# Kernel optimization log

Measured on AMD Instinct MI355X. Metric: run time of the kernel, lower is better.

## Reference

```python
import jax, jax.numpy as jnp
import numpy as np

# NF4 codebook (QLoRA): 16 quantile values of a standard normal, normalized to [-1, 1]
NF4_TABLE = jnp.array([
    -1.0, -0.6961928009986877, -0.5250730514526367, -0.39491748809814453,
    -0.28444138169288635, -0.18477343022823334, -0.09105003625154495, 0.0,
    0.07958029955625534, 0.16093020141124725, 0.24611230194568634,
    0.33791524171829224, 0.44070982933044434, 0.5626170039176941,
    0.7229568362236328, 1.0], dtype=jnp.float32)

IN_DIM = 4096
OUT_DIM = 4096
RANK = 16
ALPHA = 32.0
BLOCK = 64  # NF4 quantization block size along the flattened weight


def setup_inputs() -> dict:
    key = jax.random.key(0)
    k1, k2, k3, k4, k5 = jax.random.split(key, 5)
    x = jax.random.normal(k1, (4, 2048, IN_DIM), dtype=jnp.float32)
    # 4-bit codes into NF4_TABLE, stored unpacked as int32
    w_codes = jax.random.randint(k2, (OUT_DIM, IN_DIM), 0, 16, dtype=jnp.int32)
    # per-block absmax scales (positive)
    w_scales = jax.random.uniform(k3, (OUT_DIM, IN_DIM // BLOCK), dtype=jnp.float32) * 0.02 + 1e-3
    # lora_a: kaiming-uniform-ish scale; lora_b: nonzero for testability (original inits to zeros)
    lora_a = jax.random.normal(k4, (RANK, IN_DIM), dtype=jnp.float32) * (1.0 / np.sqrt(IN_DIM))
    lora_b = jax.random.normal(k5, (OUT_DIM, RANK), dtype=jnp.float32) * 0.01
    return {"x": x, "w_codes": w_codes, "w_scales": w_scales, "lora_a": lora_a, "lora_b": lora_b}


def _dequant_nf4(w_codes, w_scales):
    # codes [O, I] -> dequantized weight [O, I]
    w = NF4_TABLE[w_codes]                                   # [O, I]
    w = w.reshape(OUT_DIM, IN_DIM // BLOCK, BLOCK) * w_scales[:, :, None]
    return w.reshape(OUT_DIM, IN_DIM)


def reference(x, w_codes, w_scales, lora_a, lora_b):
    # base: frozen NF4 linear (dequantize then matmul), no bias
    w = _dequant_nf4(w_codes, w_scales)                      # [O, I]
    base = jnp.einsum('bsi,oi->bso', x, w)                   # [B, S, O]
    # LoRA path: dropout p=0.0 -> identity; scale alpha / rank
    ax = jnp.einsum('bsi,ri->bsr', x, lora_a)                # [B, S, r]
    lora = jnp.einsum('bsr,or->bso', ax, lora_b)             # [B, S, O]
    return base + (ALPHA / RANK) * lora
```

## Files before the change

### kernel.cpp

```cpp
#include <hip/hip_runtime.h>
#include <hip/hip_bf16.h>


#define IN_DIM  4096
#define OUT_DIM 4096
#define RANK    16
#define M_TOK   8192
#define LORA_SCALE 2.0f

typedef __bf16 bf16_t;
typedef bf16_t bf16x8 __attribute__((ext_vector_type(8)));
typedef float  f32x4  __attribute__((ext_vector_type(4)));

__device__ __constant__ float NF4_TAB[16] = {
    -1.0f, -0.6961928009986877f, -0.5250730514526367f, -0.39491748809814453f,
    -0.28444138169288635f, -0.18477343022823334f, -0.09105003625154495f, 0.0f,
    0.07958029955625534f, 0.16093020141124725f, 0.24611230194568634f,
    0.33791524171829224f, 0.44070982933044434f, 0.5626170039176941f,
    0.7229568362236328f, 1.0f};

__global__ __launch_bounds__(256) void prep_w(
    const int* __restrict__ codes, const float* __restrict__ scales,
    const float* __restrict__ la, const float* __restrict__ lb,
    bf16_t* __restrict__ W)
{
    __shared__ float nf4s[16];
    __shared__ float lbs[4][16];
    const int o0 = blockIdx.x * 4;
    const int tid = threadIdx.x;
    if (tid < 64) lbs[tid >> 4][tid & 15] = lb[(o0 + (tid >> 4)) * RANK + (tid & 15)] * LORA_SCALE;
    else if (tid < 80) nf4s[tid - 64] = NF4_TAB[tid - 64];
    __syncthreads();

    #pragma unroll
    for (int it = 0; it < 2; ++it) {
        const int i0 = (it * 256 + tid) * 8;
        float w[4][8];
        #pragma unroll
        for (int oo = 0; oo < 4; ++oo) {
            const size_t base = (size_t)(o0 + oo) * IN_DIM + i0;
            int4 c0 = *(const int4*)(codes + base);
            int4 c1 = *(const int4*)(codes + base + 4);
            const float sc = scales[(o0 + oo) * (IN_DIM / 64) + (i0 >> 6)];
            w[oo][0] = nf4s[c0.x] * sc; w[oo][1] = nf4s[c0.y] * sc;
            w[oo][2] = nf4s[c0.z] * sc; w[oo][3] = nf4s[c0.w] * sc;
            w[oo][4] = nf4s[c1.x] * sc; w[oo][5] = nf4s[c1.y] * sc;
            w[oo][6] = nf4s[c1.z] * sc; w[oo][7] = nf4s[c1.w] * sc;
        }
        #pragma unroll
        for (int r = 0; r < RANK; ++r) {
            float4 a0 = *(const float4*)(la + r * IN_DIM + i0);
            float4 a1 = *(const float4*)(la + r * IN_DIM + i0 + 4);
            #pragma unroll
            for (int oo = 0; oo < 4; ++oo) {
                const float b = lbs[oo][r];
                w[oo][0] += b * a0.x; w[oo][1] += b * a0.y;
                w[oo][2] += b * a0.z; w[oo][3] += b * a0.w;
                w[oo][4] += b * a1.x; w[oo][5] += b * a1.y;
                w[oo][6] += b * a1.z; w[oo][7] += b * a1.w;
            }
        }
        #pragma unroll
        for (int oo = 0; oo < 4; ++oo) {
            bf16x8 v;
            #pragma unroll
            for (int j = 0; j < 8; ++j) v[j] = (bf16_t)w[oo][j];
            *(bf16x8*)(W + (size_t)(o0 + oo) * IN_DIM + i0) = v;
        }
    }
}

__global__ __launch_bounds__(256) void cast_x(
    const float* __restrict__ x, bf16_t* __restrict__ y, int n8)
{
    const int stride = gridDim.x * blockDim.x;
    for (int i = blockIdx.x * blockDim.x + threadIdx.x; i < n8; i += stride) {
        const size_t e = (size_t)i * 8;
        float4 a = *(const float4*)(x + e);
        float4 b = *(const float4*)(x + e + 4);
        bf16x8 v;
        v[0] = (bf16_t)a.x; v[1] = (bf16_t)a.y; v[2] = (bf16_t)a.z; v[3] = (bf16_t)a.w;
        v[4] = (bf16_t)b.x; v[5] = (bf16_t)b.y; v[6] = (bf16_t)b.z; v[7] = (bf16_t)b.w;
        *(bf16x8*)(y + e) = v;
    }
}

__global__ __launch_bounds__(512, 2) void gemm_bt(
    const bf16_t* __restrict__ A, const bf16_t* __restrict__ B,
    float* __restrict__ C)
{
    __shared__ __align__(128) char lds[131072];

    const int tid  = threadIdx.x;
    const int wave = tid >> 6;
    const int lane = tid & 63;

    const int flat = blockIdx.y * gridDim.x + blockIdx.x;
    const int swz  = (flat & 7) * 64 + (flat >> 3);
    const int bx = swz & 15;
    const int by = swz >> 4;
    const int m0 = by * 256;
    const int n0 = bx * 256;

    const int wr = wave >> 2;
    const int wc = wave & 3;

    f32x4 acc[8][4];
    #pragma unroll
    for (int i = 0; i < 8; ++i)
        #pragma unroll
        for (int j = 0; j < 4; ++j) acc[i][j] = (f32x4)0.0f;

    const int frow = lane & 15;
    const int fch  = lane >> 4;
    const int fxor = (fch ^ ((frow >> 1) & 3)) << 4;
    const int aoff = (wr * 128 + frow) * 64 + fxor;
    const int boff = (wc * 64  + frow) * 64 + fxor;

    const int d0 = tid * 16, d1 = 8192 + tid * 16;
    const int sr0 = d0 >> 6, sr1 = d1 >> 6;
    const int sg0 = ((d0 >> 4) & 3) ^ ((sr0 >> 1) & 3);
    const int sg1 = ((d1 >> 4) & 3) ^ ((sr1 >> 1) & 3);
    const char* gA = (const char*)A;
    const char* gB = (const char*)B;

    bf16x8 fAe[8], fAo[8], fBe[2], fBo[2];

#define RD_A2(FA, SL, KH, J0) do {                                             \
    const char* b_ = lds + (SL) * 65536 + (KH) * 16384;                        \
    FA[(J0)]     = *(const bf16x8*)(b_ + aoff + (J0) * 1024);                  \
    FA[(J0) + 1] = *(const bf16x8*)(b_ + aoff + ((J0) + 1) * 1024);            \
} while (0)

#define RD_B(FB, SL, KH, NH) do {                                              \
    const char* b_ = lds + (SL) * 65536 + 32768 + (KH) * 16384;                \
    FB[0] = *(const bf16x8*)(b_ + boff + (NH) * 2048);                         \
    FB[1] = *(const bf16x8*)(b_ + boff + (NH) * 2048 + 1024);                  \
} while (0)

#define STG1(OPI, KH_, SL, T) do {                                             \
    const char* g_  = (OPI) ? gB : gA;                                         \
    const int   r0_ = (OPI) ? n0 : m0;                                         \
    const size_t ko_ = (size_t)(T) * 128 + (KH_) * 64;                         \
    const char* s0_ = g_ + (size_t)(r0_ + sr0) * 8192 + ko_ + (sg0 << 4);      \
    const char* s1_ = g_ + (size_t)(r0_ + sr1) * 8192 + ko_ + (sg1 << 4);      \
    char* db_ = lds + (SL) * 65536 + (OPI) * 32768 + (KH_) * 16384 + wave * 1024; \
    __builtin_amdgcn_global_load_lds(                                          \
        (const __attribute__((address_space(1))) void*)s0_,                    \
        (__attribute__((address_space(3))) void*)db_, 16, 0, 0);               \
    __builtin_amdgcn_global_load_lds(                                          \
        (const __attribute__((address_space(1))) void*)s1_,                    \
        (__attribute__((address_space(3))) void*)(db_ + 8192), 16, 0, 0);      \
} while (0)

#define MM4(FA, F0, FB, BI, NH) do {                                           \
    _Pragma("unroll")                                                          \
    for (int f_ = 0; f_ < 4; ++f_)                                             \
        acc[(F0) + f_][(NH) * 2 + (BI)] =                                      \
            __builtin_amdgcn_mfma_f32_16x16x32_bf16(                           \
                FA[(F0) + f_], FB[BI], acc[(F0) + f_][(NH) * 2 + (BI)], 0, 0, 0); \
} while (0)

#define PHASE(SOP, SKH, SSL, ST, CHK, FA, FB, NH, RD1, RD2, RD3) do {          \
    STG1(SOP, SKH, SSL, ST);                                                   \
    if (CHK) { asm volatile("s_waitcnt vmcnt(6)" ::: "memory"); }              \
    __builtin_amdgcn_sched_barrier(0);                                         \
    __builtin_amdgcn_s_barrier();                                              \
    __builtin_amdgcn_s_setprio(1);                                             \
    MM4(FA, 0, FB, 0, NH);                                                     \
    RD1;                                                                       \
    MM4(FA, 0, FB, 1, NH);                                                     \
    RD2;                                                                       \
    MM4(FA, 4, FB, 0, NH);                                                     \
    RD3;                                                                       \
    MM4(FA, 4, FB, 1, NH);                                                     \
    __builtin_amdgcn_s_setprio(0);                                             \
    __builtin_amdgcn_s_barrier();                                              \
} while (0)

    STG1(0, 0, 0, 0); STG1(1, 0, 0, 0); STG1(0, 1, 0, 0); STG1(1, 1, 0, 0);
    STG1(0, 0, 1, 1); STG1(1, 0, 1, 1); STG1(0, 1, 1, 1);
    asm volatile("s_waitcnt vmcnt(6)" ::: "memory");
    __builtin_amdgcn_s_barrier();
    RD_A2(fAe, 0, 0, 0); RD_A2(fAe, 0, 0, 2);
    RD_A2(fAe, 0, 0, 4); RD_A2(fAe, 0, 0, 6);
    RD_B(fBe, 0, 0, 0);

    for (int i = 0; i < 32; ++i) {
        const int tY  = 2 * i + 1;
        const int tS0 = (2 * i + 2) & 63;
        const int tS1 = (2 * i + 3) & 63;
        PHASE(1, 1, 1, tY,  0, fAe, fBe, 0,
              RD_A2(fAo, 0, 1, 0), RD_A2(fAo, 0, 1, 2), RD_B(fBo, 0, 0, 1));
        PHASE(0, 0, 0, tS0, 1, fAe, fBo, 1,
              RD_A2(fAo, 0, 1, 4), RD_A2(fAo, 0, 1, 6), RD_B(fBe, 0, 1, 0));
        PHASE(1, 0, 0, tS0, 0, fAo, fBe, 0,
              RD_A2(fAe, 1, 0, 0), RD_A2(fAe, 1, 0, 2), RD_B(fBo, 0, 1, 1));
        PHASE(0, 1, 0, tS0, 1, fAo, fBo, 1,
              RD_A2(fAe, 1, 0, 4), RD_A2(fAe, 1, 0, 6), RD_B(fBe, 1, 0, 0));
        PHASE(1, 1, 0, tS0, 0, fAe, fBe, 0,
              RD_A2(fAo, 1, 1, 0), RD_A2(fAo, 1, 1, 2), RD_B(fBo, 1, 0, 1));
        PHASE(0, 0, 1, tS1, 1, fAe, fBo, 1,
              RD_A2(fAo, 1, 1, 4), RD_A2(fAo, 1, 1, 6), RD_B(fBe, 1, 1, 0));
        PHASE(1, 0, 1, tS1, 0, fAo, fBe, 0,
              RD_A2(fAe, 0, 0, 0), RD_A2(fAe, 0, 0, 2), RD_B(fBo, 1, 1, 1));
        PHASE(0, 1, 1, tS1, 1, fAo, fBo, 1,
              RD_A2(fAe, 0, 0, 4), RD_A2(fAe, 0, 0, 6), RD_B(fBe, 0, 0, 0));
    }

    const int crow = (lane >> 4) * 4;
    const int ccol = lane & 15;
    #pragma unroll
    for (int i = 0; i < 8; ++i) {
        #pragma unroll
        for (int j = 0; j < 4; ++j) {
            const int mb = m0 + wr * 128 + i * 16 + crow;
            const int nb = n0 + wc * 64 + j * 16 + ccol;
            #pragma unroll
            for (int r = 0; r < 4; ++r)
                C[(size_t)(mb + r) * OUT_DIM + nb] = acc[i][j][r];
        }
    }
#undef RD_A2
#undef RD_B
#undef STG1
#undef MM4
#undef PHASE
}

extern "C" void kernel_launch(void* const* d_in, const int* in_sizes, int n_in,
                              void* d_out, int out_size, void* d_ws, size_t ws_size,
                              hipStream_t stream) {
    const float* x      = (const float*)d_in[0];
    const int*   codes  = (const int*)d_in[1];
    const float* scales = (const float*)d_in[2];
    const float* la     = (const float*)d_in[3];
    const float* lb     = (const float*)d_in[4];
    float* out = (float*)d_out;

    bf16_t* W  = (bf16_t*)d_ws;
    bf16_t* xb = (bf16_t*)((char*)d_ws + (size_t)OUT_DIM * IN_DIM * 2);

    prep_w<<<OUT_DIM / 4, 256, 0, stream>>>(codes, scales, la, lb, W);
    cast_x<<<2048, 256, 0, stream>>>(x, xb, (M_TOK * IN_DIM) / 8);

    dim3 grid(OUT_DIM / 256, M_TOK / 256);
    gemm_bt<<<grid, 512, 0, stream>>>(xb, W, out);
}
```

Before: 293.7 us.

## Switch GEMM to 32x32x16 MFMA and merge weight prep with x cast

The GEMM inner loop now issues 32x32x16 bf16 MFMAs into 16-wide accumulators instead of 16x16x32 tiles, which changes the LDS fragment addressing and the output store mapping. The aim is fewer MFMA issues and better operand reuse per instruction. Separately, the NF4 weight dequant/LoRA-fold kernel and the x-to-bf16 cast are merged into one launch so they share the GPU and one launch overhead is dropped. The main risks are a wrong fragment or k-ordering mapping for the larger MFMA, and coalescing changes in the store epilogue.

```diff
diff --git a/kernel.cpp b/kernel.cpp
--- a/kernel.cpp
+++ b/kernel.cpp
@@ -9,8 +9,8 @@
 #define LORA_SCALE 2.0f
 
 typedef __bf16 bf16_t;
-typedef bf16_t bf16x8 __attribute__((ext_vector_type(8)));
-typedef float  f32x4  __attribute__((ext_vector_type(4)));
+typedef bf16_t bf16x8  __attribute__((ext_vector_type(8)));
+typedef float  f32x16  __attribute__((ext_vector_type(16)));
 
 __device__ __constant__ float NF4_TAB[16] = {
     -1.0f, -0.6961928009986877f, -0.5250730514526367f, -0.39491748809814453f,
@@ -19,69 +19,70 @@
     0.33791524171829224f, 0.44070982933044434f, 0.5626170039176941f,
     0.7229568362236328f, 1.0f};
 
-__global__ __launch_bounds__(256) void prep_w(
+__global__ __launch_bounds__(256) void prep_all(
+    const float* __restrict__ x,
     const int* __restrict__ codes, const float* __restrict__ scales,
     const float* __restrict__ la, const float* __restrict__ lb,
-    bf16_t* __restrict__ W)
+    bf16_t* __restrict__ W, bf16_t* __restrict__ xb)
 {
-    __shared__ float nf4s[16];
-    __shared__ float lbs[4][16];
-    const int o0 = blockIdx.x * 4;
     const int tid = threadIdx.x;
-    if (tid < 64) lbs[tid >> 4][tid & 15] = lb[(o0 + (tid >> 4)) * RANK + (tid & 15)] * LORA_SCALE;
-    else if (tid < 80) nf4s[tid - 64] = NF4_TAB[tid - 64];
-    __syncthreads();
-
-    #pragma unroll
-    for (int it = 0; it < 2; ++it) {
-        const int i0 = (it * 256 + tid) * 8;
-        float w[4][8];
+    if (blockIdx.x < 1024) {
+        __shared__ float nf4s[16];
+        __shared__ float lbs[4][16];
+        const int o0 = blockIdx.x * 4;
+        if (tid < 64) lbs[tid >> 4][tid & 15] = lb[(o0 + (tid >> 4)) * RANK + (tid & 15)] * LORA_SCALE;
+        else if (tid < 80) nf4s[tid - 64] = NF4_TAB[tid - 64];
+        __syncthreads();
+
         #pragma unroll
-        for (int oo = 0; oo < 4; ++oo) {
-            const size_t base = (size_t)(o0 + oo) * IN_DIM + i0;
-            int4 c0 = *(const int4*)(codes + base);
-            int4 c1 = *(const int4*)(codes + base + 4);
-            const float sc = scales[(o0 + oo) * (IN_DIM / 64) + (i0 >> 6)];
-            w[oo][0] = nf4s[c0.x] * sc; w[oo][1] = nf4s[c0.y] * sc;
-            w[oo][2] = nf4s[c0.z] * sc; w[oo][3] = nf4s[c0.w] * sc;
-            w[oo][4] = nf4s[c1.x] * sc; w[oo][5] = nf4s[c1.y] * sc;
-            w[oo][6] = nf4s[c1.z] * sc; w[oo][7] = nf4s[c1.w] * sc;
+        for (int it = 0; it < 2; ++it) {
+            const int i0 = (it * 256 + tid) * 8;
+            float w[4][8];
+            #pragma unroll
+            for (int oo = 0; oo < 4; ++oo) {
+                const size_t base = (size_t)(o0 + oo) * IN_DIM + i0;
+                int4 c0 = *(const int4*)(codes + base);
+                int4 c1 = *(const int4*)(codes + base + 4);
+                const float sc = scales[(o0 + oo) * (IN_DIM / 64) + (i0 >> 6)];
+                w[oo][0] = nf4s[c0.x] * sc; w[oo][1] = nf4s[c0.y] * sc;
+                w[oo][2] = nf4s[c0.z] * sc; w[oo][3] = nf4s[c0.w] * sc;
+                w[oo][4] = nf4s[c1.x] * sc; w[oo][5] = nf4s[c1.y] * sc;
+                w[oo][6] = nf4s[c1.z] * sc; w[oo][7] = nf4s[c1.w] * sc;
+            }
+            #pragma unroll
+            for (int r = 0; r < RANK; ++r) {
+                float4 a0 = *(const float4*)(la + r * IN_DIM + i0);
+                float4 a1 = *(const float4*)(la + r * IN_DIM + i0 + 4);
+                #pragma unroll
+                for (int oo = 0; oo < 4; ++oo) {
+                    const float b = lbs[oo][r];
+                    w[oo][0] += b * a0.x; w[oo][1] += b * a0.y;
+                    w[oo][2] += b * a0.z; w[oo][3] += b * a0.w;
+                    w[oo][4] += b * a1.x; w[oo][5] += b * a1.y;
+                    w[oo][6] += b * a1.z; w[oo][7] += b * a1.w;
+                }
+            }
+            #pragma unroll
+            for (int oo = 0; oo < 4; ++oo) {
+                bf16x8 v;
+                #pragma unroll
+                for (int j = 0; j < 8; ++j) v[j] = (bf16_t)w[oo][j];
+                *(bf16x8*)(W + (size_t)(o0 + oo) * IN_DIM + i0) = v;
+            }
         }
-        #pragma unroll
-        for (int r = 0; r < RANK; ++r) {
-            float4 a0 = *(const float4*)(la + r * IN_DIM + i0);
-            float4 a1 = *(const float4*)(la + r * IN_DIM + i0 + 4);
-            #pragma unroll
-            for (int oo = 0; oo < 4; ++oo) {
-                const float b = lbs[oo][r];
-                w[oo][0] += b * a0.x; w[oo][1] += b * a0.y;
-                w[oo][2] += b * a0.z; w[oo][3] += b * a0.w;
-                w[oo][4] += b * a1.x; w[oo][5] += b * a1.y;
-                w[oo][6] += b * a1.z; w[oo][7] += b * a1.w;
-            }
+    } else {
+        const int bid = blockIdx.x - 1024;
+        const int n8 = (M_TOK * IN_DIM) / 8;
+        const int stride = 2048 * 256;
+        for (int i = bid * 256 + tid; i < n8; i += stride) {
+            const size_t e = (size_t)i * 8;
+            float4 a = *(const float4*)(x + e);
+            float4 b = *(const float4*)(x + e + 4);
+            bf16x8 v;
+            v[0] = (bf16_t)a.x; v[1] = (bf16_t)a.y; v[2] = (bf16_t)a.z; v[3] = (bf16_t)a.w;
+            v[4] = (bf16_t)b.x; v[5] = (bf16_t)b.y; v[6] = (bf16_t)b.z; v[7] = (bf16_t)b.w;
+            *(bf16x8*)(xb + e) = v;
         }
-        #pragma unroll
-        for (int oo = 0; oo < 4; ++oo) {
-            bf16x8 v;
-            #pragma unroll
-            for (int j = 0; j < 8; ++j) v[j] = (bf16_t)w[oo][j];
-            *(bf16x8*)(W + (size_t)(o0 + oo) * IN_DIM + i0) = v;
-        }
-    }
-}
-
-__global__ __launch_bounds__(256) void cast_x(
-    const float* __restrict__ x, bf16_t* __restrict__ y, int n8)
-{
-    const int stride = gridDim.x * blockDim.x;
-    for (int i = blockIdx.x * blockDim.x + threadIdx.x; i < n8; i += stride) {
-        const size_t e = (size_t)i * 8;
-        float4 a = *(const float4*)(x + e);
-        float4 b = *(const float4*)(x + e + 4);
-        bf16x8 v;
-        v[0] = (bf16_t)a.x; v[1] = (bf16_t)a.y; v[2] = (bf16_t)a.z; v[3] = (bf16_t)a.w;
-        v[4] = (bf16_t)b.x; v[5] = (bf16_t)b.y; v[6] = (bf16_t)b.z; v[7] = (bf16_t)b.w;
-        *(bf16x8*)(y + e) = v;
     }
 }
 
@@ -105,17 +106,19 @@
     const int wr = wave >> 2;
     const int wc = wave & 3;
 
-    f32x4 acc[8][4];
+    f32x16 acc[4][2];
     #pragma unroll
-    for (int i = 0; i < 8; ++i)
+    for (int i = 0; i < 4; ++i)
         #pragma unroll
-        for (int j = 0; j < 4; ++j) acc[i][j] = (f32x4)0.0f;
-
-    const int frow = lane & 15;
-    const int fch  = lane >> 4;
-    const int fxor = (fch ^ ((frow >> 1) & 3)) << 4;
-    const int aoff = (wr * 128 + frow) * 64 + fxor;
-    const int boff = (wc * 64  + frow) * 64 + fxor;
+        for (int j = 0; j < 2; ++j) acc[i][j] = (f32x16)0.0f;
+
+    const int l31  = lane & 31;
+    const int hi   = lane >> 5;
+    const int xorv = (l31 >> 1) & 3;
+    const int cs0  = ((0 + hi) ^ xorv) << 4;
+    const int cs1  = ((2 + hi) ^ xorv) << 4;
+    const int base_a = (wr * 128 + l31) * 64;
+    const int base_b = (wc * 64  + l31) * 64;
 
     const int d0 = tid * 16, d1 = 8192 + tid * 16;
     const int sr0 = d0 >> 6, sr1 = d1 >> 6;
@@ -127,15 +130,17 @@
     bf16x8 fAe[8], fAo[8], fBe[2], fBo[2];
 
 #define RD_A2(FA, SL, KH, J0) do {                                             \
-    const char* b_ = lds + (SL) * 65536 + (KH) * 16384;                        \
-    FA[(J0)]     = *(const bf16x8*)(b_ + aoff + (J0) * 1024);                  \
-    FA[(J0) + 1] = *(const bf16x8*)(b_ + aoff + ((J0) + 1) * 1024);            \
+    const char* b_ = lds + (SL) * 65536 + (KH) * 16384 + base_a               \
+                     + ((J0) >> 1) * 2048;                                     \
+    FA[(J0)]     = *(const bf16x8*)(b_ + cs0);                                 \
+    FA[(J0) + 1] = *(const bf16x8*)(b_ + cs1);                                 \
 } while (0)
 
 #define RD_B(FB, SL, KH, NH) do {                                              \
-    const char* b_ = lds + (SL) * 65536 + 32768 + (KH) * 16384;                \
-    FB[0] = *(const bf16x8*)(b_ + boff + (NH) * 2048);                         \
-    FB[1] = *(const bf16x8*)(b_ + boff + (NH) * 2048 + 1024);                  \
+    const char* b_ = lds + (SL) * 65536 + 32768 + (KH) * 16384 + base_b       \
+                     + (NH) * 2048;                                            \
+    FB[0] = *(const bf16x8*)(b_ + cs0);                                        \
+    FB[1] = *(const bf16x8*)(b_ + cs1);                                        \
 } while (0)
 
 #define STG1(OPI, KH_, SL, T) do {                                             \
@@ -153,12 +158,11 @@
         (__attribute__((address_space(3))) void*)(db_ + 8192), 16, 0, 0);      \
 } while (0)
 
-#define MM4(FA, F0, FB, BI, NH) do {                                           \
-    _Pragma("unroll")                                                          \
-    for (int f_ = 0; f_ < 4; ++f_)                                             \
-        acc[(F0) + f_][(NH) * 2 + (BI)] =                                      \
-            __builtin_amdgcn_mfma_f32_16x16x32_bf16(                           \
-                FA[(F0) + f_], FB[BI], acc[(F0) + f_][(NH) * 2 + (BI)], 0, 0, 0); \
+#define MM2(FA, FB, I, NH) do {                                                \
+    acc[I][NH] = __builtin_amdgcn_mfma_f32_32x32x16_bf16(                      \
+        FA[2 * (I)], FB[0], acc[I][NH], 0, 0, 0);                              \
+    acc[I][NH] = __builtin_amdgcn_mfma_f32_32x32x16_bf16(                      \
+        FA[2 * (I) + 1], FB[1], acc[I][NH], 0, 0, 0);                          \
 } while (0)
 
 #define PHASE(SOP, SKH, SSL, ST, CHK, FA, FB, NH, RD1, RD2, RD3) do {          \
@@ -167,13 +171,13 @@
     __builtin_amdgcn_sched_barrier(0);                                         \
     __builtin_amdgcn_s_barrier();                                              \
     __builtin_amdgcn_s_setprio(1);                                             \
-    MM4(FA, 0, FB, 0, NH);                                                     \
+    MM2(FA, FB, 0, NH);                                                        \
     RD1;                                                                       \
-    MM4(FA, 0, FB, 1, NH);                                                     \
+    MM2(FA, FB, 1, NH);                                                        \
     RD2;                                                                       \
-    MM4(FA, 4, FB, 0, NH);                                                     \
+    MM2(FA, FB, 2, NH);                                                        \
     RD3;                                                                       \
-    MM4(FA, 4, FB, 1, NH);                                                     \
+    MM2(FA, FB, 3, NH);                                                        \
     __builtin_amdgcn_s_setprio(0);                                             \
     __builtin_amdgcn_s_barrier();                                              \
 } while (0)
@@ -208,23 +212,23 @@
               RD_A2(fAe, 0, 0, 4), RD_A2(fAe, 0, 0, 6), RD_B(fBe, 0, 0, 0));
     }
 
-    const int crow = (lane >> 4) * 4;
-    const int ccol = lane & 15;
     #pragma unroll
-    for (int i = 0; i < 8; ++i) {
+    for (int i = 0; i < 4; ++i) {
         #pragma unroll
-        for (int j = 0; j < 4; ++j) {
-            const int mb = m0 + wr * 128 + i * 16 + crow;
-            const int nb = n0 + wc * 64 + j * 16 + ccol;
-            #pragma unroll
-            for (int r = 0; r < 4; ++r)
-                C[(size_t)(mb + r) * OUT_DIM + nb] = acc[i][j][r];
+        for (int j = 0; j < 2; ++j) {
+            const int mb = m0 + wr * 128 + i * 32 + 4 * hi;
+            const int nb = n0 + wc * 64 + j * 32 + l31;
+            #pragma unroll
+            for (int reg = 0; reg < 16; ++reg) {
+                const int row = (reg & 3) + 8 * (reg >> 2);
+                C[(size_t)(mb + row) * OUT_DIM + nb] = acc[i][j][reg];
+            }
         }
     }
 #undef RD_A2
 #undef RD_B
 #undef STG1
-#undef MM4
+#undef MM2
 #undef PHASE
 }
 
@@ -241,8 +245,7 @@
     bf16_t* W  = (bf16_t*)d_ws;
     bf16_t* xb = (bf16_t*)((char*)d_ws + (size_t)OUT_DIM * IN_DIM * 2);
 
-    prep_w<<<OUT_DIM / 4, 256, 0, stream>>>(codes, scales, la, lb, W);
-    cast_x<<<2048, 256, 0, stream>>>(x, xb, (M_TOK * IN_DIM) / 8);
+    prep_all<<<1024 + 2048, 256, 0, stream>>>(x, codes, scales, la, lb, W, xb);
 
     dim3 grid(OUT_DIM / 256, M_TOK / 256);
     gemm_bt<<<grid, 512, 0, stream>>>(xb, W, out);
```

After: 305.8 us. +4.1%, slower.
